# Optimization experiments

Hardware: AMD Instinct MI355X
Metric: run time of the kernel (lower is better)

The kernel has to match this reference:

```python
import jax, jax.numpy as jnp
import numpy as np

H = 50   # hidden_size
D = 8    # input_size
B = 2048
T = 512


def setup_inputs() -> dict:
    key = jax.random.key(0)
    ks = jax.random.split(key, 11)
    s = 1.0 / np.sqrt(H)  # PyTorch LSTM/Linear default init bound
    u = lambda k, shape: jax.random.uniform(k, shape, jnp.float32, -s, s)
    return {
        "x": jax.random.normal(ks[0], (B, T, D), jnp.float32),
        # layer 0: input 8 -> hidden 50 (gate order i,f,g,o as in PyTorch)
        "Wih0": u(ks[1], (4 * H, D)),
        "Whh0": u(ks[2], (4 * H, H)),
        "bih0": u(ks[3], (4 * H,)),
        "bhh0": u(ks[4], (4 * H,)),
        # layer 1: hidden 50 -> hidden 50
        "Wih1": u(ks[5], (4 * H, H)),
        "Whh1": u(ks[6], (4 * H, H)),
        "bih1": u(ks[7], (4 * H,)),
        "bhh1": u(ks[8], (4 * H,)),
        # final linear 50 -> 1
        "Wlin": u(ks[9], (1, H)),
        "blin": u(ks[10], (1,)),
    }


def _lstm_layer(x, Wih, Whh, b):
    # x: [B, T, Din] -> outputs h over time: [B, T, H]
    Bb = x.shape[0]
    Hh = Whh.shape[1]
    # precompute input-to-gate projection for all timesteps (one big GEMM)
    x_proj = jnp.einsum("btd,gd->btg", x, Wih) + b  # [B, T, 4H]

    def step(carry, xt):
        h, c = carry
        gates = xt + h @ Whh.T  # [B, 4H]
        i, f, g, o = jnp.split(gates, 4, axis=-1)
        i = jax.nn.sigmoid(i)
        f = jax.nn.sigmoid(f)
        g = jnp.tanh(g)
        o = jax.nn.sigmoid(o)
        c = f * c + i * g
        h = o * jnp.tanh(c)
        return (h, c), h

    init = (jnp.zeros((Bb, Hh), x.dtype), jnp.zeros((Bb, Hh), x.dtype))
    _, hs = jax.lax.scan(step, init, jnp.swapaxes(x_proj, 0, 1))  # [T, B, H]
    return jnp.swapaxes(hs, 0, 1)


def reference(x, Wih0, Whh0, bih0, bhh0, Wih1, Whh1, bih1, bhh1, Wlin, blin):
    h1 = _lstm_layer(x, Wih0, Whh0, bih0 + bhh0)   # [B, T, H]
    h2 = _lstm_layer(h1, Wih1, Whh1, bih1 + bhh1)  # [B, T, H]
    last = h2[:, -1, :]                            # [B, H]
    return last @ Wlin.T + blin                    # [B, 1]
```

## Files before the change

kernel.cpp:

```cpp
#include <hip/hip_runtime.h>
#include <math.h>

#define Hn 50
#define Dn 8
#define Tn 512
#define BB 8
#define NBLK 256
#define KST 136

typedef __attribute__((ext_vector_type(8))) short short8;
typedef __attribute__((ext_vector_type(4))) float f32x4;

__device__ __forceinline__ float fexp2_(float x) {
#if __has_builtin(__builtin_amdgcn_exp2f)
    return __builtin_amdgcn_exp2f(x);
#else
    return exp2f(x);
#endif
}
__device__ __forceinline__ float frcp_(float x) {
#if __has_builtin(__builtin_amdgcn_rcpf)
    return __builtin_amdgcn_rcpf(x);
#else
    return 1.0f / x;
#endif
}
__device__ __forceinline__ float sigmoidf_(float x) {
    return frcp_(1.0f + fexp2_(-1.44269504f * x));
}
__device__ __forceinline__ float tanhf_(float x) {
    return 2.0f * sigmoidf_(2.0f * x) - 1.0f;
}
__device__ __forceinline__ float bf2f(short s) {
    return __uint_as_float(((unsigned)(unsigned short)s) << 16);
}
__device__ __forceinline__ void split_bf(float v, short& hi, short& lo) {
    hi = (short)(__float_as_uint(v) >> 16);
    const float r = v - bf2f(hi);
    lo = (short)(__float_as_uint(r) >> 16);
}
__device__ __forceinline__ float lstm_cell4(const f32x4 g4, float& c) {
    c = sigmoidf_(g4.y) * c + sigmoidf_(g4.x) * tanhf_(g4.z);
    return sigmoidf_(g4.w) * tanhf_(c);
}
__device__ __forceinline__ float shflxor8(float v) {
    return __shfl_xor(v, 8, 64);
}


template<int NL1, int NL0, bool XD>
__device__ __forceinline__ void run_loop(
    const int* l1T, const int* l0T,
    int b0, int lane, int quad, int col,
    short (*bP)[16][KST], float* h1f, const float* x,
    const float* Wih0, const float* Whh0, const float* bih0, const float* bhh0,
    const float* Wih1, const float* Whh1, const float* bih1, const float* bhh1)
{
    constexpr int NS = NL1 + NL0;
    constexpr int NPAIR = (NS + 1) / 2;
    constexpr int NBF = (NL1 > 0) ? 4 : 2;

    short8 W1[NL1 > 0 ? NL1 : 1][4][2];
    short8 W0[NL0 > 0 ? NL0 : 1][2][2];
    float  bias[NS][4];
    int    kb[NS];
    int    cellb[NS];

    #pragma unroll
    for (int i = 0; i < NL1; ++i) {
        const int T = l1T[i];
        const int ng = T * 16 + col, cl = ng >> 2, g = ng & 3;
        const bool on = (cl < Hn);
        const int grow = g * Hn + cl;
        #pragma unroll
        for (int s = 0; s < 4; ++s)
            #pragma unroll
            for (int j = 0; j < 8; ++j) {
                const int k = 32 * s + quad * 8 + j;
                float v = 0.f;
                if (on) {
                    if (k < Hn)                      v = Wih1[grow * Hn + k];
                    else if (k >= 64 && k < 64 + Hn) v = Whh1[grow * Hn + (k - 64)];
                }
                short hi, lo; split_bf(v, hi, lo);
                W1[i][s][0][j] = hi; W1[i][s][1][j] = lo;
            }
        const int myc = 4 * T + quad;
        #pragma unroll
        for (int r = 0; r < 4; ++r)
            bias[i][r] = (myc < Hn) ? (bih1[r * Hn + myc] + bhh1[r * Hn + myc]) : 0.f;
        kb[i] = 64 + 4 * T; cellb[i] = 4 * T;
    }
    #pragma unroll
    for (int i = 0; i < NL0; ++i) {
        const int T = l0T[i];
        const int ng = T * 16 + col, cl = ng >> 2, g = ng & 3;
        const bool on = (cl < Hn);
        const int grow = g * Hn + cl;
        #pragma unroll
        for (int s = 0; s < 2; ++s)
            #pragma unroll
            for (int j = 0; j < 8; ++j) {
                const int k = 32 * s + quad * 8 + j;
                float v = 0.f;
                if (on) {
                    if (k < Hn)           v = Whh0[grow * Hn + k];
                    else if (k < Hn + Dn) v = Wih0[grow * Dn + (k - Hn)];
                }
                short hi, lo; split_bf(v, hi, lo);
                W0[i][s][0][j] = hi; W0[i][s][1][j] = lo;
            }
        const int myc = 4 * T + quad;
        #pragma unroll
        for (int r = 0; r < 4; ++r)
            bias[NL1 + i][r] = (myc < Hn) ? (bih0[r * Hn + myc] + bhh0[r * Hn + myc]) : 0.f;
        kb[NL1 + i] = 4 * T; cellb[NL1 + i] = 4 * T;
    }

    float c[NPAIR];
    #pragma unroll
    for (int p = 0; p < NPAIR; ++p) c[p] = 0.f;

    const float* xp = XD ? (x + (size_t)(b0 + (lane >> 3)) * Tn * Dn + (lane & 7))
                         : (const float*)nullptr;

    for (int t = 0; t < Tn; ++t) {
        float xv = 0.f;
        if (XD) { if (t + 1 < Tn) xv = xp[(size_t)(t + 1) * Dn]; }

        const short (*bR)[KST] = (const short (*)[KST])bP[t & 1];
        short (*bW)[KST] = bP[(t + 1) & 1];

        short8 BF[NBF];
        #pragma unroll
        for (int s = 0; s < NBF; ++s)
            BF[s] = *(const short8*)&bR[col][32 * s + quad * 8];

        f32x4 acc[NS];
        #pragma unroll
        for (int i = 0; i < NS; ++i) {
            #pragma unroll
            for (int r = 0; r < 4; ++r) acc[i][r] = (col < 8) ? bias[i][r] : 0.f;
        }
        #pragma unroll
        for (int i = 0; i < NL1; ++i)
            #pragma unroll
            for (int s = 0; s < 4; ++s) {
                acc[i] = __builtin_amdgcn_mfma_f32_16x16x32_bf16(W1[i][s][0], BF[s], acc[i], 0, 0, 0);
                acc[i] = __builtin_amdgcn_mfma_f32_16x16x32_bf16(W1[i][s][1], BF[s], acc[i], 0, 0, 0);
            }
        #pragma unroll
        for (int i = 0; i < NL0; ++i)
            #pragma unroll
            for (int s = 0; s < 2; ++s) {
                acc[NL1 + i] = __builtin_amdgcn_mfma_f32_16x16x32_bf16(W0[i][s][0], BF[s], acc[NL1 + i], 0, 0, 0);
                acc[NL1 + i] = __builtin_amdgcn_mfma_f32_16x16x32_bf16(W0[i][s][1], BF[s], acc[NL1 + i], 0, 0, 0);
            }

        #pragma unroll
        for (int p = 0; p < NPAIR; ++p) {
            const int ia = 2 * p;
            const bool hasB  = (ia + 1 < NS);
            const bool isL1a = (ia < NL1);
            const bool isL1b = (ia + 1 < NL1);
            f32x4 g;
            #pragma unroll
            for (int r = 0; r < 4; ++r) {
                const float sa = acc[ia][r] + shflxor8(acc[ia][r]);
                float sel = sa;
                if (hasB) {
                    const float sb = acc[ia + 1][r] + shflxor8(acc[ia + 1][r]);
                    sel = (col < 8) ? sa : sb;
                }
                g[r] = sel;
            }
            int cell, kc; bool isl1;
            if (hasB && col >= 8) { cell = cellb[ia + 1] + quad; kc = kb[ia + 1] + quad; isl1 = isL1b; }
            else                  { cell = cellb[ia] + quad;     kc = kb[ia] + quad;     isl1 = isL1a; }
            const bool doAct = (cell < Hn) && ((t >= 1) || !isl1);
            if (doAct) {
                const float h = lstm_cell4(g, c[p]);
                short hi, lo; split_bf(h, hi, lo);
                if (hasB) { bW[col & 7][kc] = hi; bW[(col & 7) + 8][kc] = lo; }
                else      { bW[col][kc] = (col < 8) ? hi : lo; }
            }
        }
        if (XD) {
            if (t + 1 < Tn) {
                short hi, lo; split_bf(xv, hi, lo);
                bW[lane >> 3][Hn + (lane & 7)]       = hi;
                bW[(lane >> 3) + 8][Hn + (lane & 7)] = lo;
            }
        }
        __syncthreads();
    }

    if constexpr (NL1 > 0) {
        const short (*bR)[KST] = (const short (*)[KST])bP[Tn & 1];
        short8 BF[4];
        #pragma unroll
        for (int s = 0; s < 4; ++s)
            BF[s] = *(const short8*)&bR[col][32 * s + quad * 8];
        f32x4 accE[NL1];
        #pragma unroll
        for (int i = 0; i < NL1; ++i) {
            #pragma unroll
            for (int r = 0; r < 4; ++r) accE[i][r] = (col < 8) ? bias[i][r] : 0.f;
        }
        #pragma unroll
        for (int i = 0; i < NL1; ++i)
            #pragma unroll
            for (int s = 0; s < 4; ++s) {
                accE[i] = __builtin_amdgcn_mfma_f32_16x16x32_bf16(W1[i][s][0], BF[s], accE[i], 0, 0, 0);
                accE[i] = __builtin_amdgcn_mfma_f32_16x16x32_bf16(W1[i][s][1], BF[s], accE[i], 0, 0, 0);
            }
        #pragma unroll
        for (int p = 0; p < NPAIR; ++p) {
            const int ia = 2 * p;
            if (ia < NL1) {
                const bool bL1 = (ia + 1 < NL1);
                f32x4 g;
                #pragma unroll
                for (int r = 0; r < 4; ++r) {
                    const float sa = accE[ia][r] + shflxor8(accE[ia][r]);
                    float sel = sa;
                    if (bL1) {
                        const float sb = accE[ia + 1][r] + shflxor8(accE[ia + 1][r]);
                        sel = (col < 8) ? sa : sb;
                    }
                    g[r] = sel;
                }
                int cell; bool mine;
                if (bL1) { cell = ((col < 8) ? cellb[ia] : cellb[ia + 1]) + quad; mine = true; }
                else     { cell = cellb[ia] + quad;                               mine = (col < 8); }
                if (mine && cell < Hn) {
                    const float h = lstm_cell4(g, c[p]);
                    h1f[cell * 8 + (col & 7)] = h;
                }
            }
        }
    }
}

__global__ __launch_bounds__(512, 1) void lstm2_kernel(
    const float* __restrict__ x,
    const float* __restrict__ Wih0, const float* __restrict__ Whh0,
    const float* __restrict__ bih0, const float* __restrict__ bhh0,
    const float* __restrict__ Wih1, const float* __restrict__ Whh1,
    const float* __restrict__ bih1, const float* __restrict__ bhh1,
    const float* __restrict__ Wlin, const float* __restrict__ blin,
    float* __restrict__ out)
{
    const int tid  = threadIdx.x;
    const int b0   = blockIdx.x * BB;
    const int w    = __builtin_amdgcn_readfirstlane(tid >> 6);
    const int lane = tid & 63;
    const int quad = lane >> 4;
    const int col  = lane & 15;

    __shared__ __align__(16) short bP[2][16][KST];
    __shared__ float h1f[Hn * 8];

    for (int i = tid; i < 2 * 16 * KST; i += 512) (&bP[0][0][0])[i] = 0;
    __syncthreads();
    if (tid < 64) {
        const int xb = tid >> 3, xd = tid & 7;
        const float f = x[((size_t)(b0 + xb) * Tn + 0) * Dn + xd];
        short hi, lo; split_bf(f, hi, lo);
        bP[0][xb][Hn + xd]     = hi;
        bP[0][xb + 8][Hn + xd] = lo;
    }
    __syncthreads();

    if (w < 6) {
        const int l1t[2] = {2 * w, 2 * w + 1};
        const int l0t[1] = {w};
        run_loop<2, 1, false>(l1t, l0t, b0, lane, quad, col, bP, h1f, x,
                              Wih0, Whh0, bih0, bhh0, Wih1, Whh1, bih1, bhh1);
    } else if (w == 6) {
        const int l1t[1] = {0};
        const int l0t[4] = {6, 7, 8, 9};
        run_loop<0, 4, true>(l1t, l0t, b0, lane, quad, col, bP, h1f, x,
                             Wih0, Whh0, bih0, bhh0, Wih1, Whh1, bih1, bhh1);
    } else {
        const int l1t[1] = {12};
        const int l0t[3] = {10, 11, 12};
        run_loop<1, 3, false>(l1t, l0t, b0, lane, quad, col, bP, h1f, x,
                              Wih0, Whh0, bih0, bhh0, Wih1, Whh1, bih1, bhh1);
    }
    __syncthreads();

    if (tid < BB) {
        float o = blin[0];
        #pragma unroll
        for (int k = 0; k < Hn; ++k) o += Wlin[k] * h1f[k * 8 + tid];
        out[b0 + tid] = o;
    }
}

extern "C" void kernel_launch(void* const* d_in, const int* in_sizes, int n_in,
                              void* d_out, int out_size, void* d_ws, size_t ws_size,
                              hipStream_t stream) {
    const float* x    = (const float*)d_in[0];
    const float* Wih0 = (const float*)d_in[1];
    const float* Whh0 = (const float*)d_in[2];
    const float* bih0 = (const float*)d_in[3];
    const float* bhh0 = (const float*)d_in[4];
    const float* Wih1 = (const float*)d_in[5];
    const float* Whh1 = (const float*)d_in[6];
    const float* bih1 = (const float*)d_in[7];
    const float* bhh1 = (const float*)d_in[8];
    const float* Wlin = (const float*)d_in[9];
    const float* blin = (const float*)d_in[10];
    float* out = (float*)d_out;

    lstm2_kernel<<<NBLK, 512, 0, stream>>>(x, Wih0, Whh0, bih0, bhh0,
                                           Wih1, Whh1, bih1, bhh1,
                                           Wlin, blin, out);
}
```

Baseline: 476.2 us.

## Split layer-0 and layer-1 tiles onto separate waves, cheapen gate reduction

Reassigns the per-wave work so waves 0-3 handle only layer-0 tiles and waves 4-7 only layer-1 tiles, instead of mixing both layers in every wave. It also rewrites the paired-tile cross-lane reduction to use one shuffle per element instead of two, and raises the launch bounds hint to two blocks per CU. The intent is to shorten the per-step critical path and allow more occupancy. The cost is some load imbalance between the waves, plus possible register pressure from the tighter launch bound, which could cause spills.

```diff
diff --git a/kernel.cpp b/kernel.cpp
--- a/kernel.cpp
+++ b/kernel.cpp
@@ -166,13 +166,13 @@
             f32x4 g;
             #pragma unroll
             for (int r = 0; r < 4; ++r) {
-                const float sa = acc[ia][r] + shflxor8(acc[ia][r]);
-                float sel = sa;
                 if (hasB) {
-                    const float sb = acc[ia + 1][r] + shflxor8(acc[ia + 1][r]);
-                    sel = (col < 8) ? sa : sb;
-                }
-                g[r] = sel;
+                    const float u = (col < 8) ? acc[ia][r]     : acc[ia + 1][r];
+                    const float v = (col < 8) ? acc[ia + 1][r] : acc[ia][r];
+                    g[r] = u + shflxor8(v);
+                } else {
+                    g[r] = acc[ia][r] + shflxor8(acc[ia][r]);
+                }
             }
             int cell, kc; bool isl1;
             if (hasB && col >= 8) { cell = cellb[ia + 1] + quad; kc = kb[ia + 1] + quad; isl1 = isL1b; }
@@ -222,13 +222,13 @@
                 f32x4 g;
                 #pragma unroll
                 for (int r = 0; r < 4; ++r) {
-                    const float sa = accE[ia][r] + shflxor8(accE[ia][r]);
-                    float sel = sa;
                     if (bL1) {
-                        const float sb = accE[ia + 1][r] + shflxor8(accE[ia + 1][r]);
-                        sel = (col < 8) ? sa : sb;
+                        const float u = (col < 8) ? accE[ia][r]     : accE[ia + 1][r];
+                        const float v = (col < 8) ? accE[ia + 1][r] : accE[ia][r];
+                        g[r] = u + shflxor8(v);
+                    } else {
+                        g[r] = accE[ia][r] + shflxor8(accE[ia][r]);
                     }
-                    g[r] = sel;
                 }
                 int cell; bool mine;
                 if (bL1) { cell = ((col < 8) ? cellb[ia] : cellb[ia + 1]) + quad; mine = true; }
@@ -242,7 +242,7 @@
     }
 }
 
-__global__ __launch_bounds__(512, 1) void lstm2_kernel(
+__global__ __launch_bounds__(512, 2) void lstm2_kernel(
     const float* __restrict__ x,
     const float* __restrict__ Wih0, const float* __restrict__ Whh0,
     const float* __restrict__ bih0, const float* __restrict__ bhh0,
@@ -272,20 +272,29 @@
     }
     __syncthreads();
 
-    if (w < 6) {
-        const int l1t[2] = {2 * w, 2 * w + 1};
-        const int l0t[1] = {w};
-        run_loop<2, 1, false>(l1t, l0t, b0, lane, quad, col, bP, h1f, x,
-                              Wih0, Whh0, bih0, bhh0, Wih1, Whh1, bih1, bhh1);
-    } else if (w == 6) {
-        const int l1t[1] = {0};
-        const int l0t[4] = {6, 7, 8, 9};
-        run_loop<0, 4, true>(l1t, l0t, b0, lane, quad, col, bP, h1f, x,
+    if (w == 0) {
+        const int l0t[4] = {0, 1, 2, 3};
+        run_loop<0, 4, false>(nullptr, l0t, b0, lane, quad, col, bP, h1f, x,
+                              Wih0, Whh0, bih0, bhh0, Wih1, Whh1, bih1, bhh1);
+    } else if (w == 1) {
+        const int l0t[3] = {4, 5, 6};
+        run_loop<0, 3, false>(nullptr, l0t, b0, lane, quad, col, bP, h1f, x,
+                              Wih0, Whh0, bih0, bhh0, Wih1, Whh1, bih1, bhh1);
+    } else if (w == 2) {
+        const int l0t[3] = {7, 8, 9};
+        run_loop<0, 3, false>(nullptr, l0t, b0, lane, quad, col, bP, h1f, x,
+                              Wih0, Whh0, bih0, bhh0, Wih1, Whh1, bih1, bhh1);
+    } else if (w == 3) {
+        const int l0t[3] = {10, 11, 12};
+        run_loop<0, 3, true>(nullptr, l0t, b0, lane, quad, col, bP, h1f, x,
                              Wih0, Whh0, bih0, bhh0, Wih1, Whh1, bih1, bhh1);
+    } else if (w == 7) {
+        const int l1t[4] = {9, 10, 11, 12};
+        run_loop<4, 0, false>(l1t, nullptr, b0, lane, quad, col, bP, h1f, x,
+                              Wih0, Whh0, bih0, bhh0, Wih1, Whh1, bih1, bhh1);
     } else {
-        const int l1t[1] = {12};
-        const int l0t[3] = {10, 11, 12};
-        run_loop<1, 3, false>(l1t, l0t, b0, lane, quad, col, bP, h1f, x,
+        const int l1t[3] = {3 * (w - 4), 3 * (w - 4) + 1, 3 * (w - 4) + 2};
+        run_loop<3, 0, false>(l1t, nullptr, b0, lane, quad, col, bP, h1f, x,
                               Wih0, Whh0, bih0, bhh0, Wih1, Whh1, bih1, bhh1);
     }
     __syncthreads();
```

After: 471.1 us. Within noise of the previous version (-1.1%).
